# Performance work log

Hardware: AMD Instinct MI355X
Metric: run time of the kernel (lower is better)

The kernel has to match this reference:

```python
import jax, jax.numpy as jnp
import numpy as np

EPS = 1.0  # Shapelet eps
STRIDE = 1


def _shapelet(x, w, pcm):
    """x: (b,c,t), w: (n,c,l), pcm: (c,m). Returns ((b, n*c) probs, (b, n*c) dists)."""
    n, c, l = w.shape
    t = x.shape[-1]
    m = (t - l) // STRIDE + 1
    # unfold: gather overlapping windows -> (b, c, m, l)
    idx = jnp.arange(m)[:, None] * STRIDE + jnp.arange(l)[None, :]
    win = x[:, :, idx]                                   # (b, c, m, l)
    xw = jnp.transpose(win, (0, 2, 1, 3))[:, :, None]    # (b, m, 1, c, l)
    d = jnp.mean(jnp.abs(xw - w), axis=-1)               # (b, m, n, c)
    d = d * pcm.T[None, :, None, :]                      # penalty (1, m, 1, c)
    p = jnp.exp(-jnp.square(EPS * d))                    # (b, m, n, c)
    hard = jax.nn.one_hot(jnp.argmax(p, axis=1), m, axis=1, dtype=p.dtype)  # (b,m,n,c)
    soft = jax.nn.softmax(p, axis=1)
    onehot_max = hard + soft - jax.lax.stop_gradient(soft)  # straight-through
    max_p = jnp.sum(onehot_max * p, axis=1)              # (b, n, c)
    d_min = jnp.min(d, axis=1)                           # (b, n, c)
    b = x.shape[0]
    return max_p.reshape(b, -1), d_min.reshape(b, -1)


def _diversity(w):
    """w: (n,c,l) -> scalar. torch PairwiseDistance(p=2, eps=1e-6) adds eps to diff."""
    sh = jnp.transpose(w, (1, 0, 2))                     # (c, n, l)
    diff = sh[:, None, :, :] - sh[:, :, None, :] + 1e-6
    dist = jnp.sqrt(jnp.sum(jnp.square(diff), axis=-1))  # (c, n, n)
    nsh = sh.shape[1]
    mask = 1.0 - jnp.eye(nsh, dtype=w.dtype)
    return jnp.mean(jnp.exp(-dist) * mask[None])


def setup_inputs() -> dict:
    key = jax.random.key(0)
    ks = jax.random.split(key, 6)
    b, c, t, ncls = 32, 8, 512, 10
    sls = [52, 103, 154, 256]
    ms = [t - l + 1 for l in sls]
    inp = {"x": jax.random.normal(ks[0], (b, c, t), dtype=jnp.float32)}
    for i, (l, m) in enumerate(zip(sls, ms)):
        inp[f"w{i}"] = jax.random.normal(ks[1 + i], (5, c, l), dtype=jnp.float32)
        inp[f"pcm{i}"] = jnp.ones((c, m), dtype=jnp.float32)
    inp["W_out"] = jax.random.normal(ks[5], (ncls, 160), dtype=jnp.float32) * 0.05
    return inp


def reference(x, w0, w1, w2, w3, pcm0, pcm1, pcm2, pcm3, W_out):
    # instance norm over time (torch std is unbiased, ddof=1)
    mu = jnp.mean(x, axis=-1, keepdims=True)
    sd = jnp.std(x, axis=-1, keepdims=True, ddof=1)
    xn = (x - mu) / (sd + 1e-8)

    ws = (w0, w1, w2, w3)
    pcms = (pcm0, pcm1, pcm2, pcm3)
    probs, dists = [], []
    for w, pcm in zip(ws, pcms):
        p, d = _shapelet(xn, w, pcm)
        probs.append(p)
        dists.append(d)
    shapelet_probs = jnp.concatenate(probs, axis=-1)   # (b, 160)
    shapelet_dists = jnp.concatenate(dists, axis=-1)   # (b, 160)

    # dropout is identity in eval mode
    out = shapelet_probs @ W_out.T                     # (b, num_classes)

    loss_reg = jnp.mean(jnp.abs(W_out))
    loss_div = sum(_diversity(w) for w in ws)
    loss = (0.1 * loss_reg + 0.1 * loss_div).reshape(1)
    return out, shapelet_dists, shapelet_probs, loss
```

## Files before the change

kernel.cpp:

```cpp
#include <hip/hip_runtime.h>
#include <math.h>

#define B 32
#define C 8
#define T 512
#define NSH 5
#define NCLS 10
#define NFEAT 160

#define OUT_OFF    0
#define DIST_OFF   (B * NCLS)
#define PROB_OFF   (DIST_OFF + B * NFEAT)
#define LOSS_OFF   (PROB_OFF + B * NFEAT)


template<int L, int M, int GOFF>
__device__ __forceinline__ void shapelet_task(
    const float* __restrict__ x,
    const float* __restrict__ wrow,
    const float* __restrict__ pmrow,
    float* __restrict__ out, int bc, int n)
{
    const int lane = threadIdx.x & 63;
    const int b = bc >> 3, c = bc & 7;
    const float* xrow = x + bc * T;

    const float4 u0 = *(const float4*)(xrow + lane * 4);
    const float4 u1 = *(const float4*)(xrow + 256 + lane * 4);
    float s = u0.x + u0.y + u0.z + u0.w + u1.x + u1.y + u1.z + u1.w;
    #pragma unroll
    for (int off = 32; off; off >>= 1) s += __shfl_down(s, off);
    const float mu = __shfl(s, 0) * (1.0f / T);
    float sq = (u0.x-mu)*(u0.x-mu) + (u0.y-mu)*(u0.y-mu) + (u0.z-mu)*(u0.z-mu) + (u0.w-mu)*(u0.w-mu)
             + (u1.x-mu)*(u1.x-mu) + (u1.y-mu)*(u1.y-mu) + (u1.z-mu)*(u1.z-mu) + (u1.w-mu)*(u1.w-mu);
    #pragma unroll
    for (int off = 32; off; off >>= 1) sq += __shfl_down(sq, off);
    const float var = __shfl(sq, 0) * (1.0f / (T - 1));
    const float ns = 1.0f / (sqrtf(var) + 1e-8f);
    const float nb = -mu * ns;

    const int sbase = lane * 8;
    const int sb = (sbase < M) ? sbase : 0;

    float4 a  = *(const float4*)(xrow + sb);
    float4 bb = *(const float4*)(xrow + sb + 4);
    float4 cc = *(const float4*)(xrow + sb + 8);
    a.x = fmaf(a.x, ns, nb);  a.y = fmaf(a.y, ns, nb);  a.z = fmaf(a.z, ns, nb);  a.w = fmaf(a.w, ns, nb);
    bb.x = fmaf(bb.x, ns, nb); bb.y = fmaf(bb.y, ns, nb); bb.z = fmaf(bb.z, ns, nb); bb.w = fmaf(bb.w, ns, nb);
    cc.x = fmaf(cc.x, ns, nb); cc.y = fmaf(cc.y, ns, nb); cc.z = fmaf(cc.z, ns, nb); cc.w = fmaf(cc.w, ns, nb);

    float acc[8] = {0,0,0,0,0,0,0,0};
    constexpr int LC = L & ~3;

    #pragma unroll 4
    for (int j = 0; j + 4 <= L; j += 4) {
        const float wa = wrow[j], wb = wrow[j+1], wc = wrow[j+2], wd = wrow[j+3];
        acc[0]+=fabsf(a.x-wa); acc[1]+=fabsf(a.y-wa); acc[2]+=fabsf(a.z-wa); acc[3]+=fabsf(a.w-wa);
        acc[4]+=fabsf(bb.x-wa); acc[5]+=fabsf(bb.y-wa); acc[6]+=fabsf(bb.z-wa); acc[7]+=fabsf(bb.w-wa);
        acc[0]+=fabsf(a.y-wb); acc[1]+=fabsf(a.z-wb); acc[2]+=fabsf(a.w-wb); acc[3]+=fabsf(bb.x-wb);
        acc[4]+=fabsf(bb.y-wb); acc[5]+=fabsf(bb.z-wb); acc[6]+=fabsf(bb.w-wb); acc[7]+=fabsf(cc.x-wb);
        acc[0]+=fabsf(a.z-wc); acc[1]+=fabsf(a.w-wc); acc[2]+=fabsf(bb.x-wc); acc[3]+=fabsf(bb.y-wc);
        acc[4]+=fabsf(bb.z-wc); acc[5]+=fabsf(bb.w-wc); acc[6]+=fabsf(cc.x-wc); acc[7]+=fabsf(cc.y-wc);
        acc[0]+=fabsf(a.w-wd); acc[1]+=fabsf(bb.x-wd); acc[2]+=fabsf(bb.y-wd); acc[3]+=fabsf(bb.z-wd);
        acc[4]+=fabsf(bb.w-wd); acc[5]+=fabsf(cc.x-wd); acc[6]+=fabsf(cc.y-wd); acc[7]+=fabsf(cc.z-wd);
        a = bb; bb = cc;
        int nidx = sb + j + 12;
        nidx = (nidx > T - 4) ? (T - 4) : nidx;
        cc = *(const float4*)(xrow + nidx);
        cc.x = fmaf(cc.x, ns, nb); cc.y = fmaf(cc.y, ns, nb);
        cc.z = fmaf(cc.z, ns, nb); cc.w = fmaf(cc.w, ns, nb);
    }

    if constexpr ((L & 3) != 0) {
        const float rr[12] = {a.x,a.y,a.z,a.w, bb.x,bb.y,bb.z,bb.w, cc.x,cc.y,cc.z,cc.w};
        #pragma unroll
        for (int jt = 0; jt < (L & 3); ++jt) {
            const float wj = wrow[LC + jt];
            #pragma unroll
            for (int k = 0; k < 8; ++k) acc[k] += fabsf(rr[jt + k] - wj);
        }
    }

    constexpr float invL = 1.0f / (float)L;
    float mind = INFINITY, mind2 = INFINITY;
    #pragma unroll
    for (int k = 0; k < 8; ++k) {
        const int m = sbase + k;
        if (m < M) {
            const float d = acc[k] * invL * pmrow[m];
            mind  = fminf(mind, d);
            mind2 = fminf(mind2, d * d);
        }
    }
    #pragma unroll
    for (int off = 32; off; off >>= 1) {
        mind  = fminf(mind,  __shfl_down(mind,  off));
        mind2 = fminf(mind2, __shfl_down(mind2, off));
    }
    if (lane == 0) {
        const int col = GOFF + n * C + c;
        out[DIST_OFF + b * NFEAT + col] = mind;
        out[PROB_OFF + b * NFEAT + col] = expf(-mind2);
    }
}

__global__ __launch_bounds__(256) void shapelet_kernel(
    const float* __restrict__ x,
    const float* __restrict__ w0, const float* __restrict__ w1,
    const float* __restrict__ w2, const float* __restrict__ w3,
    const float* __restrict__ p0, const float* __restrict__ p1,
    const float* __restrict__ p2, const float* __restrict__ p3,
    const float* __restrict__ Wout,
    float* __restrict__ out, float* __restrict__ wsf)
{
    const int blk = blockIdx.x;
    const int wv  = __builtin_amdgcn_readfirstlane(threadIdx.x >> 6);

    if (blk < 1280) {
        const int bc = blk / 5;
        const int gn = (blk - bc * 5) * 4 + wv;
        const int g  = gn / 5;
        const int n  = gn - g * 5;
        const int c  = bc & 7;
        switch (g) {
            case 0: shapelet_task< 52, 461,   0>(x, w0 + (n*C+c)*52,  p0 + c*461, out, bc, n); break;
            case 1: shapelet_task<103, 410,  40>(x, w1 + (n*C+c)*103, p1 + c*410, out, bc, n); break;
            case 2: shapelet_task<154, 359,  80>(x, w2 + (n*C+c)*154, p2 + c*359, out, bc, n); break;
            default:shapelet_task<256, 257, 120>(x, w3 + (n*C+c)*256, p3 + c*257, out, bc, n); break;
        }
    } else if (blk < 1440) {
        const int task = (blk - 1280) * 4 + wv;
        const int lane = threadIdx.x & 63;
        const int g  = task / 160;
        const int r  = task - g * 160;
        const int c  = r / 20;
        const int pr = r - c * 20;
        const int i  = pr >> 2;
        const int j0 = pr & 3;
        const int j  = j0 + (j0 >= i ? 1 : 0);
        const float* wptrs[4] = { w0, w1, w2, w3 };
        const int    Ls[4]    = { 52, 103, 154, 256 };
        const int L = Ls[g];
        const float* wi = wptrs[g] + (i * C + c) * L;
        const float* wj = wptrs[g] + (j * C + c) * L;
        float ss = 0.0f;
        for (int t2 = lane; t2 < L; t2 += 64) {
            const float df = wj[t2] - wi[t2] + 1e-6f;
            ss += df * df;
        }
        #pragma unroll
        for (int off = 32; off; off >>= 1) ss += __shfl_down(ss, off);
        if (lane == 0) wsf[task] = expf(-sqrtf(ss));
    } else {
        const int lane = threadIdx.x & 63;
        float rg = 0.0f;
        #pragma unroll
        for (int k2 = 0; k2 < 7; ++k2) {
            const int e = lane + k2 * 64;
            if (e < 400) rg += fabsf(Wout[wv * 400 + e]);
        }
        #pragma unroll
        for (int off = 32; off; off >>= 1) rg += __shfl_down(rg, off);
        if (lane == 0) wsf[640 + wv] = rg;
    }
}

__global__ __launch_bounds__(64) void head_kernel(
    const float* __restrict__ Wout,
    const float* __restrict__ wsf,
    float* __restrict__ out)
{
    const int blk  = blockIdx.x;
    const int lane = threadIdx.x;
    if (blk < B * NCLS) {
        const int b = blk / NCLS, k = blk - b * NCLS;
        const float* pr = out + PROB_OFF + b * NFEAT;
        const float* wr = Wout + k * NFEAT;
        float acc = 0.0f;
        #pragma unroll
        for (int r = 0; r < 3; ++r) {
            const int f = lane + r * 64;
            if (f < NFEAT) acc += pr[f] * wr[f];
        }
        #pragma unroll
        for (int off = 32; off; off >>= 1) acc += __shfl_down(acc, off);
        if (lane == 0) out[OUT_OFF + blk] = acc;
    } else {
        float dv = 0.0f, rg = 0.0f;
        #pragma unroll
        for (int r = 0; r < 10; ++r) {
            const int i = lane + r * 64;
            if (i < 640) dv += wsf[i];
        }
        if (lane < 4) rg = wsf[640 + lane];
        #pragma unroll
        for (int off = 32; off; off >>= 1) {
            dv += __shfl_down(dv, off);
            rg += __shfl_down(rg, off);
        }
        if (lane == 0)
            out[LOSS_OFF] = 0.1f * (rg * (1.0f / 1600.0f)) + 0.1f * (dv * (1.0f / 200.0f));
    }
}

extern "C" void kernel_launch(void* const* d_in, const int* in_sizes, int n_in,
                              void* d_out, int out_size, void* d_ws, size_t ws_size,
                              hipStream_t stream) {
    const float* x    = (const float*)d_in[0];
    const float* w0   = (const float*)d_in[1];
    const float* pcm0 = (const float*)d_in[2];
    const float* w1   = (const float*)d_in[3];
    const float* pcm1 = (const float*)d_in[4];
    const float* w2   = (const float*)d_in[5];
    const float* pcm2 = (const float*)d_in[6];
    const float* w3   = (const float*)d_in[7];
    const float* pcm3 = (const float*)d_in[8];
    const float* Wout = (const float*)d_in[9];
    float* out = (float*)d_out;
    float* wsf = (float*)d_ws;

    shapelet_kernel<<<1441, 256, 0, stream>>>(
        x, w0, w1, w2, w3, pcm0, pcm1, pcm2, pcm3, Wout, out, wsf);
    head_kernel<<<B * NCLS + 1, 64, 0, stream>>>(Wout, wsf, out);
}
```

Baseline: 111.4 us.

## Restructure shapelet distances: pre-normalize x, transpose weights, per-lane windows with partial mins

Adds a prep kernel that instance-normalizes x once into a padded workspace buffer and transposes shapelet weights so all 5 shapelets of a channel sit together for each offset. The main kernel now gives each lane one window position and accumulates distances to all 5 shapelets at once, reusing each x value across shapelets. Each wave writes partial min values per chunk of positions. The head kernel reduces those partials, computes probs and the output matmul through shared memory. This removes redundant normalization and per-shapelet reloads of x, at the cost of an extra launch, workspace round trips and uniform weight loads per lane.

```diff
diff --git a/kernel.cpp b/kernel.cpp
--- a/kernel.cpp
+++ b/kernel.cpp
@@ -13,124 +13,53 @@
 #define PROB_OFF   (DIST_OFF + B * NFEAT)
 #define LOSS_OFF   (PROB_OFF + B * NFEAT)
 
-
-template<int L, int M, int GOFF>
-__device__ __forceinline__ void shapelet_task(
-    const float* __restrict__ x,
-    const float* __restrict__ wrow,
-    const float* __restrict__ pmrow,
-    float* __restrict__ out, int bc, int n)
-{
-    const int lane = threadIdx.x & 63;
-    const int b = bc >> 3, c = bc & 7;
-    const float* xrow = x + bc * T;
-
-    const float4 u0 = *(const float4*)(xrow + lane * 4);
-    const float4 u1 = *(const float4*)(xrow + 256 + lane * 4);
-    float s = u0.x + u0.y + u0.z + u0.w + u1.x + u1.y + u1.z + u1.w;
-    #pragma unroll
-    for (int off = 32; off; off >>= 1) s += __shfl_down(s, off);
-    const float mu = __shfl(s, 0) * (1.0f / T);
-    float sq = (u0.x-mu)*(u0.x-mu) + (u0.y-mu)*(u0.y-mu) + (u0.z-mu)*(u0.z-mu) + (u0.w-mu)*(u0.w-mu)
-             + (u1.x-mu)*(u1.x-mu) + (u1.y-mu)*(u1.y-mu) + (u1.z-mu)*(u1.z-mu) + (u1.w-mu)*(u1.w-mu);
-    #pragma unroll
-    for (int off = 32; off; off >>= 1) sq += __shfl_down(sq, off);
-    const float var = __shfl(sq, 0) * (1.0f / (T - 1));
-    const float ns = 1.0f / (sqrtf(var) + 1e-8f);
-    const float nb = -mu * ns;
-
-    const int sbase = lane * 8;
-    const int sb = (sbase < M) ? sbase : 0;
-
-    float4 a  = *(const float4*)(xrow + sb);
-    float4 bb = *(const float4*)(xrow + sb + 4);
-    float4 cc = *(const float4*)(xrow + sb + 8);
-    a.x = fmaf(a.x, ns, nb);  a.y = fmaf(a.y, ns, nb);  a.z = fmaf(a.z, ns, nb);  a.w = fmaf(a.w, ns, nb);
-    bb.x = fmaf(bb.x, ns, nb); bb.y = fmaf(bb.y, ns, nb); bb.z = fmaf(bb.z, ns, nb); bb.w = fmaf(bb.w, ns, nb);
-    cc.x = fmaf(cc.x, ns, nb); cc.y = fmaf(cc.y, ns, nb); cc.z = fmaf(cc.z, ns, nb); cc.w = fmaf(cc.w, ns, nb);
-
-    float acc[8] = {0,0,0,0,0,0,0,0};
-    constexpr int LC = L & ~3;
-
-    #pragma unroll 4
-    for (int j = 0; j + 4 <= L; j += 4) {
-        const float wa = wrow[j], wb = wrow[j+1], wc = wrow[j+2], wd = wrow[j+3];
-        acc[0]+=fabsf(a.x-wa); acc[1]+=fabsf(a.y-wa); acc[2]+=fabsf(a.z-wa); acc[3]+=fabsf(a.w-wa);
-        acc[4]+=fabsf(bb.x-wa); acc[5]+=fabsf(bb.y-wa); acc[6]+=fabsf(bb.z-wa); acc[7]+=fabsf(bb.w-wa);
-        acc[0]+=fabsf(a.y-wb); acc[1]+=fabsf(a.z-wb); acc[2]+=fabsf(a.w-wb); acc[3]+=fabsf(bb.x-wb);
-        acc[4]+=fabsf(bb.y-wb); acc[5]+=fabsf(bb.z-wb); acc[6]+=fabsf(bb.w-wb); acc[7]+=fabsf(cc.x-wb);
-        acc[0]+=fabsf(a.z-wc); acc[1]+=fabsf(a.w-wc); acc[2]+=fabsf(bb.x-wc); acc[3]+=fabsf(bb.y-wc);
-        acc[4]+=fabsf(bb.z-wc); acc[5]+=fabsf(bb.w-wc); acc[6]+=fabsf(cc.x-wc); acc[7]+=fabsf(cc.y-wc);
-        acc[0]+=fabsf(a.w-wd); acc[1]+=fabsf(bb.x-wd); acc[2]+=fabsf(bb.y-wd); acc[3]+=fabsf(bb.z-wd);
-        acc[4]+=fabsf(bb.w-wd); acc[5]+=fabsf(cc.x-wd); acc[6]+=fabsf(cc.y-wd); acc[7]+=fabsf(cc.z-wd);
-        a = bb; bb = cc;
-        int nidx = sb + j + 12;
-        nidx = (nidx > T - 4) ? (T - 4) : nidx;
-        cc = *(const float4*)(xrow + nidx);
-        cc.x = fmaf(cc.x, ns, nb); cc.y = fmaf(cc.y, ns, nb);
-        cc.z = fmaf(cc.z, ns, nb); cc.w = fmaf(cc.w, ns, nb);
-    }
-
-    if constexpr ((L & 3) != 0) {
-        const float rr[12] = {a.x,a.y,a.z,a.w, bb.x,bb.y,bb.z,bb.w, cc.x,cc.y,cc.z,cc.w};
-        #pragma unroll
-        for (int jt = 0; jt < (L & 3); ++jt) {
-            const float wj = wrow[LC + jt];
-            #pragma unroll
-            for (int k = 0; k < 8; ++k) acc[k] += fabsf(rr[jt + k] - wj);
-        }
-    }
-
-    constexpr float invL = 1.0f / (float)L;
-    float mind = INFINITY, mind2 = INFINITY;
-    #pragma unroll
-    for (int k = 0; k < 8; ++k) {
-        const int m = sbase + k;
-        if (m < M) {
-            const float d = acc[k] * invL * pmrow[m];
-            mind  = fminf(mind, d);
-            mind2 = fminf(mind2, d * d);
-        }
-    }
-    #pragma unroll
-    for (int off = 32; off; off >>= 1) {
-        mind  = fminf(mind,  __shfl_down(mind,  off));
-        mind2 = fminf(mind2, __shfl_down(mind2, off));
-    }
-    if (lane == 0) {
-        const int col = GOFF + n * C + c;
-        out[DIST_OFF + b * NFEAT + col] = mind;
-        out[PROB_OFF + b * NFEAT + col] = expf(-mind2);
-    }
-}
-
-__global__ __launch_bounds__(256) void shapelet_kernel(
+#define XN_OFF   1024
+#define XSTRIDE  520
+#define WT0_OFF  140000
+#define WT1_OFF  142080
+#define WT2_OFF  146200
+#define WT3_OFF  152360
+#define P3_OFF   200000
+#define P2_OFF   212800
+#define P1_OFF   228160
+#define P0_OFF   246080
+
+__global__ __launch_bounds__(256) void prep_kernel(
     const float* __restrict__ x,
     const float* __restrict__ w0, const float* __restrict__ w1,
     const float* __restrict__ w2, const float* __restrict__ w3,
-    const float* __restrict__ p0, const float* __restrict__ p1,
-    const float* __restrict__ p2, const float* __restrict__ p3,
     const float* __restrict__ Wout,
-    float* __restrict__ out, float* __restrict__ wsf)
+    float* __restrict__ wsf)
 {
-    const int blk = blockIdx.x;
-    const int wv  = __builtin_amdgcn_readfirstlane(threadIdx.x >> 6);
-
-    if (blk < 1280) {
-        const int bc = blk / 5;
-        const int gn = (blk - bc * 5) * 4 + wv;
-        const int g  = gn / 5;
-        const int n  = gn - g * 5;
-        const int c  = bc & 7;
-        switch (g) {
-            case 0: shapelet_task< 52, 461,   0>(x, w0 + (n*C+c)*52,  p0 + c*461, out, bc, n); break;
-            case 1: shapelet_task<103, 410,  40>(x, w1 + (n*C+c)*103, p1 + c*410, out, bc, n); break;
-            case 2: shapelet_task<154, 359,  80>(x, w2 + (n*C+c)*154, p2 + c*359, out, bc, n); break;
-            default:shapelet_task<256, 257, 120>(x, w3 + (n*C+c)*256, p3 + c*257, out, bc, n); break;
-        }
-    } else if (blk < 1440) {
-        const int task = (blk - 1280) * 4 + wv;
-        const int lane = threadIdx.x & 63;
+    const int blk  = blockIdx.x;
+    const int tid  = threadIdx.x;
+    const int wv   = __builtin_amdgcn_readfirstlane(tid >> 6);
+    const int lane = tid & 63;
+
+    if (blk < 64) {
+        const int bc = blk * 4 + wv;
+        const float* xr = x + bc * T;
+        const float4 u0 = *(const float4*)(xr + lane * 4);
+        const float4 u1 = *(const float4*)(xr + 256 + lane * 4);
+        float s = u0.x + u0.y + u0.z + u0.w + u1.x + u1.y + u1.z + u1.w;
+        #pragma unroll
+        for (int off = 32; off; off >>= 1) s += __shfl_down(s, off);
+        const float mu = __shfl(s, 0) * (1.0f / T);
+        float sq = (u0.x-mu)*(u0.x-mu) + (u0.y-mu)*(u0.y-mu) + (u0.z-mu)*(u0.z-mu) + (u0.w-mu)*(u0.w-mu)
+                 + (u1.x-mu)*(u1.x-mu) + (u1.y-mu)*(u1.y-mu) + (u1.z-mu)*(u1.z-mu) + (u1.w-mu)*(u1.w-mu);
+        #pragma unroll
+        for (int off = 32; off; off >>= 1) sq += __shfl_down(sq, off);
+        const float var = __shfl(sq, 0) * (1.0f / (T - 1));
+        const float ns  = 1.0f / (sqrtf(var) + 1e-8f);
+        const float nbv = -mu * ns;
+        float* xo = wsf + XN_OFF + bc * XSTRIDE;
+        const float4 o0 = { fmaf(u0.x,ns,nbv), fmaf(u0.y,ns,nbv), fmaf(u0.z,ns,nbv), fmaf(u0.w,ns,nbv) };
+        const float4 o1 = { fmaf(u1.x,ns,nbv), fmaf(u1.y,ns,nbv), fmaf(u1.z,ns,nbv), fmaf(u1.w,ns,nbv) };
+        *(float4*)(xo + lane * 4)       = o0;
+        *(float4*)(xo + 256 + lane * 4) = o1;
+        if (lane < 2) *(float4*)(xo + T + lane * 4) = float4{0.f, 0.f, 0.f, 0.f};
+    } else if (blk < 224) {
+        const int task = (blk - 64) * 4 + wv;
         const int g  = task / 160;
         const int r  = task - g * 160;
         const int c  = r / 20;
@@ -151,8 +80,7 @@
         #pragma unroll
         for (int off = 32; off; off >>= 1) ss += __shfl_down(ss, off);
         if (lane == 0) wsf[task] = expf(-sqrtf(ss));
-    } else {
-        const int lane = threadIdx.x & 63;
+    } else if (blk == 224) {
         float rg = 0.0f;
         #pragma unroll
         for (int k2 = 0; k2 < 7; ++k2) {
@@ -162,36 +90,196 @@
         #pragma unroll
         for (int off = 32; off; off >>= 1) rg += __shfl_down(rg, off);
         if (lane == 0) wsf[640 + wv] = rg;
-    }
-}
-
-__global__ __launch_bounds__(64) void head_kernel(
+    } else {
+        const int e = (blk - 225) * 256 + tid;
+        if (e < 2080) {
+            constexpr int L = 52;
+            const int c = e / (L*5), r2 = e % (L*5), j = r2 / 5, n = r2 % 5;
+            wsf[WT0_OFF + e] = w0[(n*C + c)*L + j];
+        } else if (e < 6200) {
+            constexpr int L = 103;
+            const int e2 = e - 2080;
+            const int c = e2 / (L*5), r2 = e2 % (L*5), j = r2 / 5, n = r2 % 5;
+            wsf[WT1_OFF + e2] = w1[(n*C + c)*L + j];
+        } else if (e < 12360) {
+            constexpr int L = 154;
+            const int e2 = e - 6200;
+            const int c = e2 / (L*5), r2 = e2 % (L*5), j = r2 / 5, n = r2 % 5;
+            wsf[WT2_OFF + e2] = w2[(n*C + c)*L + j];
+        } else if (e < 22600) {
+            constexpr int L = 256;
+            const int e2 = e - 12360;
+            const int c = e2 / (L*5), r2 = e2 % (L*5), j = r2 / 5, n = r2 % 5;
+            wsf[WT3_OFF + e2] = w3[(n*C + c)*L + j];
+        }
+    }
+}
+
+template<int L, int M, int S>
+__device__ __forceinline__ void shapelet_task_p(
+    const float* __restrict__ xn,
+    const float* __restrict__ wt,
+    const float* __restrict__ pmg,
+    float* __restrict__ part,
+    int r)
+{
+    const int lane = threadIdx.x & 63;
+    const int bc = r / S;
+    const int ms = r - bc * S;
+    const int c  = bc & 7;
+    const int m  = ms * 64 + lane;
+    const bool act = (m < M);
+    const int mm = act ? m : 0;
+    const float* xr = xn + bc * XSTRIDE + mm;
+    const float* wp = wt + c * (L * 5);
+
+    float a0 = 0, a1 = 0, a2 = 0, a3 = 0, a4 = 0;
+
+    float xf[8];
+    #pragma unroll
+    for (int q = 0; q < 8; ++q) xf[q] = xr[q];
+
+    constexpr int NB  = L / 8;
+    constexpr int REM = L % 8;
+    for (int it = 0; it < NB; ++it) {
+        const int j = it * 8;
+        float cw[40];
+        #pragma unroll
+        for (int q = 0; q < 40; ++q) cw[q] = wp[j * 5 + q];
+        float nxf[8];
+        #pragma unroll
+        for (int q = 0; q < 8; ++q) nxf[q] = xr[j + 8 + q];
+        #pragma unroll
+        for (int jj = 0; jj < 8; ++jj) {
+            const float xv = xf[jj];
+            a0 += fabsf(xv - cw[jj*5+0]);
+            a1 += fabsf(xv - cw[jj*5+1]);
+            a2 += fabsf(xv - cw[jj*5+2]);
+            a3 += fabsf(xv - cw[jj*5+3]);
+            a4 += fabsf(xv - cw[jj*5+4]);
+        }
+        #pragma unroll
+        for (int q = 0; q < 8; ++q) xf[q] = nxf[q];
+    }
+    if constexpr (REM > 0) {
+        constexpr int j = NB * 8;
+        float cw[REM * 5];
+        #pragma unroll
+        for (int q = 0; q < REM * 5; ++q) cw[q] = wp[j * 5 + q];
+        #pragma unroll
+        for (int jj = 0; jj < REM; ++jj) {
+            const float xv = xf[jj];
+            a0 += fabsf(xv - cw[jj*5+0]);
+            a1 += fabsf(xv - cw[jj*5+1]);
+            a2 += fabsf(xv - cw[jj*5+2]);
+            a3 += fabsf(xv - cw[jj*5+3]);
+            a4 += fabsf(xv - cw[jj*5+4]);
+        }
+    }
+
+    const float pmv = pmg[c * M + mm];
+    constexpr float invL = 1.0f / (float)L;
+    const float scale = invL * pmv;
+
+    float dv[5], d2[5];
+    dv[0] = act ? a0 * scale : INFINITY;
+    dv[1] = act ? a1 * scale : INFINITY;
+    dv[2] = act ? a2 * scale : INFINITY;
+    dv[3] = act ? a3 * scale : INFINITY;
+    dv[4] = act ? a4 * scale : INFINITY;
+    #pragma unroll
+    for (int n = 0; n < 5; ++n) d2[n] = act ? dv[n] * dv[n] : INFINITY;
+
+    #pragma unroll
+    for (int off = 32; off; off >>= 1) {
+        #pragma unroll
+        for (int n = 0; n < 5; ++n) {
+            dv[n] = fminf(dv[n], __shfl_down(dv[n], off));
+            d2[n] = fminf(d2[n], __shfl_down(d2[n], off));
+        }
+    }
+    if (lane == 0) {
+        #pragma unroll
+        for (int n = 0; n < 5; ++n) {
+            float* p = part + ((bc * 5 + n) * S + ms) * 2;
+            p[0] = dv[n];
+            p[1] = d2[n];
+        }
+    }
+}
+
+__global__ __launch_bounds__(256) void shapelet_kernel(
+    const float* __restrict__ p0, const float* __restrict__ p1,
+    const float* __restrict__ p2, const float* __restrict__ p3,
+    float* __restrict__ wsf)
+{
+    const int wv = __builtin_amdgcn_readfirstlane(threadIdx.x >> 6);
+    const int wt = blockIdx.x * 4 + wv;
+    const float* xn = wsf + XN_OFF;
+
+    if (wt < 1280)
+        shapelet_task_p<256, 257, 5>(xn, wsf + WT3_OFF, p3, wsf + P3_OFF, wt);
+    else if (wt < 2816)
+        shapelet_task_p<154, 359, 6>(xn, wsf + WT2_OFF, p2, wsf + P2_OFF, wt - 1280);
+    else if (wt < 4608)
+        shapelet_task_p<103, 410, 7>(xn, wsf + WT1_OFF, p1, wsf + P1_OFF, wt - 2816);
+    else
+        shapelet_task_p< 52, 461, 8>(xn, wsf + WT0_OFF, p0, wsf + P0_OFF, wt - 4608);
+}
+
+__global__ __launch_bounds__(256) void head2_kernel(
     const float* __restrict__ Wout,
     const float* __restrict__ wsf,
     float* __restrict__ out)
 {
-    const int blk  = blockIdx.x;
-    const int lane = threadIdx.x;
-    if (blk < B * NCLS) {
-        const int b = blk / NCLS, k = blk - b * NCLS;
-        const float* pr = out + PROB_OFF + b * NFEAT;
-        const float* wr = Wout + k * NFEAT;
-        float acc = 0.0f;
-        #pragma unroll
-        for (int r = 0; r < 3; ++r) {
-            const int f = lane + r * 64;
-            if (f < NFEAT) acc += pr[f] * wr[f];
-        }
-        #pragma unroll
-        for (int off = 32; off; off >>= 1) acc += __shfl_down(acc, off);
-        if (lane == 0) out[OUT_OFF + blk] = acc;
-    } else {
+    const int blk = blockIdx.x;
+    const int tid = threadIdx.x;
+
+    if (blk < B) {
+        const int b = blk;
+        __shared__ float pl[NFEAT];
+        if (tid < NFEAT) {
+            const int col = tid;
+            const int g   = col / 40;
+            const int rem = col - g * 40;
+            const int n   = rem >> 3;
+            const int c   = rem & 7;
+            const int bc  = b * C + c;
+            int S, pbase;
+            switch (g) {
+                case 0:  S = 8; pbase = P0_OFF; break;
+                case 1:  S = 7; pbase = P1_OFF; break;
+                case 2:  S = 6; pbase = P2_OFF; break;
+                default: S = 5; pbase = P3_OFF; break;
+            }
+            const float* p = wsf + pbase + ((bc * 5 + n) * S) * 2;
+            float mnd = INFINITY, mn2 = INFINITY;
+            for (int msi = 0; msi < S; ++msi) {
+                mnd = fminf(mnd, p[msi * 2]);
+                mn2 = fminf(mn2, p[msi * 2 + 1]);
+            }
+            out[DIST_OFF + b * NFEAT + col] = mnd;
+            const float pb = expf(-mn2);
+            out[PROB_OFF + b * NFEAT + col] = pb;
+            pl[col] = pb;
+        }
+        __syncthreads();
+        if (tid < NFEAT) {
+            const int k = tid >> 4, seg = tid & 15;
+            const float* wr = Wout + k * NFEAT + seg * 10;
+            const float* pp = pl + seg * 10;
+            float acc = 0.0f;
+            #pragma unroll
+            for (int q = 0; q < 10; ++q) acc += pp[q] * wr[q];
+            #pragma unroll
+            for (int off = 8; off; off >>= 1) acc += __shfl_down(acc, off, 16);
+            if (seg == 0) out[OUT_OFF + b * NCLS + k] = acc;
+        }
+    } else if (tid < 64) {
+        const int lane = tid;
         float dv = 0.0f, rg = 0.0f;
         #pragma unroll
-        for (int r = 0; r < 10; ++r) {
-            const int i = lane + r * 64;
-            if (i < 640) dv += wsf[i];
-        }
+        for (int r = 0; r < 10; ++r) dv += wsf[lane + r * 64];
         if (lane < 4) rg = wsf[640 + lane];
         #pragma unroll
         for (int off = 32; off; off >>= 1) {
@@ -219,7 +307,7 @@
     float* out = (float*)d_out;
     float* wsf = (float*)d_ws;
 
-    shapelet_kernel<<<1441, 256, 0, stream>>>(
-        x, w0, w1, w2, w3, pcm0, pcm1, pcm2, pcm3, Wout, out, wsf);
-    head_kernel<<<B * NCLS + 1, 64, 0, stream>>>(Wout, wsf, out);
-}
+    prep_kernel<<<314, 256, 0, stream>>>(x, w0, w1, w2, w3, Wout, wsf);
+    shapelet_kernel<<<1664, 256, 0, stream>>>(pcm0, pcm1, pcm2, pcm3, wsf);
+    head2_kernel<<<B + 1, 256, 0, stream>>>(Wout, wsf, out);
+}
```

Result: slower. 120.7 us (+8.4%).
